# Kernel tuning notes

Hardware: AMD Instinct MI355X
Metric: run time of the kernel (lower is better)

The kernel has to match this reference:

```python
import jax, jax.numpy as jnp
import numpy as np

QMIN, QMAX = 0.0, 255.0  # uint8 affine quantization range


def _quant_dequant(x, scale, zero_point):
    # affine static quantization: q = clamp(round(x/scale) + zp, 0, 255)
    q = jnp.clip(jnp.round(x / scale) + zero_point, QMIN, QMAX)
    # dequantize back to float for the reference GEMM
    return (q - zero_point) * scale


def setup_inputs() -> dict:
    key = jax.random.key(0)
    k1, k2, k3, k4, k5 = jax.random.split(key, 5)
    N, IN, OUT = 4096, 4096, 4096
    x = jax.random.normal(k1, (N, IN), dtype=jnp.float32)
    weight = jax.random.normal(k2, (OUT, IN), dtype=jnp.float32) * 0.02
    bias = jax.random.normal(k3, (OUT,), dtype=jnp.float32)
    # static qparams (as produced by calculate_qparams of the observers)
    act_scale = jnp.float32(4.0 * 2.0 / 255.0)  # covers ~[-4, 4]
    act_zero_point = jnp.int32(128)
    weight_scale = (jax.random.uniform(k4, (OUT,), dtype=jnp.float32) * 0.5 + 0.5) * (0.08 * 2.0 / 255.0)
    weight_zero_point = jnp.full((OUT,), 128, dtype=jnp.int32)
    return {
        "x": x,
        "weight": weight,
        "bias": bias,
        "act_scale": act_scale,
        "act_zero_point": act_zero_point,
        "weight_scale": weight_scale,
        "weight_zero_point": weight_zero_point,
    }


def reference(x, weight, bias, act_scale, act_zero_point, weight_scale, weight_zero_point):
    # per-tensor static activation quantization
    x_dq = _quant_dequant(x, act_scale, act_zero_point.astype(jnp.float32))  # [N, in]
    # per-output-row weight quantization (block_size = (1, in_features))
    w_dq = _quant_dequant(
        weight,
        weight_scale[:, None],
        weight_zero_point.astype(jnp.float32)[:, None],
    )  # [out, in]
    # F.linear: x @ W^T + b
    return jnp.einsum("ni,oi->no", x_dq, w_dq) + bias
```

## Files before the change

kernel.cpp:

```cpp
#include <hip/hip_runtime.h>
#include <stdint.h>

typedef int   int4v   __attribute__((ext_vector_type(4)));
typedef float float4v __attribute__((ext_vector_type(4)));

static constexpr int DIM = 4096;
static constexpr int BT  = 128;
static constexpr int BK  = 128;
static constexpr int NKT = DIM / BK;

__global__ __launch_bounds__(256) void quant_act_kernel(
    const float* __restrict__ x, const float* __restrict__ s_ptr,
    const int* __restrict__ zp_ptr, int* __restrict__ out, int n4) {
  const float s  = s_ptr[0];
  const int   zp = zp_ptr[0];
  int idx    = blockIdx.x * blockDim.x + threadIdx.x;
  int stride = gridDim.x * blockDim.x;
  for (int i = idx; i < n4; i += stride) {
    float4v v = reinterpret_cast<const float4v*>(x)[i];
    int packed = 0;
#pragma unroll
    for (int j = 0; j < 4; ++j) {
      int q = (int)rintf(v[j] / s) + zp;
      q = min(max(q, 0), 255);
      q -= zp;
      packed |= (q & 255) << (8 * j);
    }
    out[i] = packed;
  }
}

__global__ __launch_bounds__(256) void quant_wgt_kernel(
    const float* __restrict__ w, const float* __restrict__ ws,
    const int* __restrict__ wzp, int* __restrict__ out, int n4) {
  int idx    = blockIdx.x * blockDim.x + threadIdx.x;
  int stride = gridDim.x * blockDim.x;
  for (int i = idx; i < n4; i += stride) {
    const int row = i >> 10;
    const float s = ws[row];
    const int  zp = wzp[row];
    float4v v = reinterpret_cast<const float4v*>(w)[i];
    int packed = 0;
#pragma unroll
    for (int j = 0; j < 4; ++j) {
      int q = (int)rintf(v[j] / s) + zp;
      q = min(max(q, 0), 255);
      q -= zp;
      packed |= (q & 255) << (8 * j);
    }
    out[i] = packed;
  }
}


__global__ __launch_bounds__(256, 2) void gemm_i8_w64(
    const signed char* __restrict__ A, const signed char* __restrict__ B,
    const float* __restrict__ s_act, const float* __restrict__ w_scale,
    const float* __restrict__ bias, float* __restrict__ C) {
  extern __shared__ signed char smem[];

  const int tid  = threadIdx.x;
  const int w    = tid >> 6;
  const int lane = tid & 63;
  const int wr = w >> 1, wc = w & 1;
  const int l15 = lane & 15, lhi = lane >> 4;
  const int swk = (l15 & 7) << 4;

  const int srow = lane >> 3;
  const int scol = ((lane & 7) ^ (lane >> 3)) << 4;

  const int tileM = blockIdx.y * BT;
  const int tileN = blockIdx.x * BT;

  auto stageA = [&](int i, int t) {
    signed char* dst = smem + (t & 1) * 32768;
    const int c = 4 * w + i;
    const size_t g = (size_t)(tileM + c * 8 + srow) * DIM + (size_t)t * BK + scol;
    __builtin_amdgcn_global_load_lds(
        (const __attribute__((address_space(1))) void*)(A + g),
        (__attribute__((address_space(3))) void*)(dst + c * 1024), 16, 0, 0);
  };
  auto stageB = [&](int i, int t) {
    signed char* dst = smem + (t & 1) * 32768 + 16384;
    const int c = 4 * w + i;
    const size_t g = (size_t)(tileN + c * 8 + srow) * DIM + (size_t)t * BK + scol;
    __builtin_amdgcn_global_load_lds(
        (const __attribute__((address_space(1))) void*)(B + g),
        (__attribute__((address_space(3))) void*)(dst + c * 1024), 16, 0, 0);
  };
  auto rdA = [&](const signed char* aL, int m, int kk) -> int4v {
    const int r = wr * 64 + m * 16 + l15;
    return *(const int4v*)(aL + r * BK + ((kk * 64 + lhi * 16) ^ swk));
  };
  auto rdB = [&](const signed char* bL, int n, int kk) -> int4v {
    const int r = wc * 64 + n * 16 + l15;
    return *(const int4v*)(bL + r * BK + ((kk * 64 + lhi * 16) ^ swk));
  };

  int4v acc[4][4] = {};
  int4v af[4][2];
  int4v bf[4][2];

#pragma unroll
  for (int i = 0; i < 4; ++i) { stageA(i, 0); stageB(i, 0); }
  asm volatile("s_waitcnt vmcnt(0)" ::: "memory");
  __builtin_amdgcn_s_barrier();

  for (int kt = 0; kt < NKT; ++kt) {
    const signed char* aC = smem + (kt & 1) * 32768;
    const signed char* bC = aC + 16384;

    if (kt + 1 < NKT) {
#pragma unroll
      for (int i = 0; i < 4; ++i) { stageA(i, kt + 1); stageB(i, kt + 1); }
    }

#pragma unroll
    for (int m = 0; m < 4; ++m) { af[m][0] = rdA(aC, m, 0); af[m][1] = rdA(aC, m, 1); }
#pragma unroll
    for (int n = 0; n < 4; ++n) { bf[n][0] = rdB(bC, n, 0); bf[n][1] = rdB(bC, n, 1); }

    __builtin_amdgcn_s_setprio(1);
#pragma unroll
    for (int kk = 0; kk < 2; ++kk)
#pragma unroll
      for (int m = 0; m < 4; ++m)
#pragma unroll
        for (int n = 0; n < 4; ++n)
          acc[m][n] = __builtin_amdgcn_mfma_i32_16x16x64_i8(
              af[m][kk], bf[n][kk], acc[m][n], 0, 0, 0);
    __builtin_amdgcn_s_setprio(0);

    asm volatile("s_waitcnt vmcnt(0)" ::: "memory");
    __builtin_amdgcn_s_barrier();
  }

  const float sa = s_act[0];
#pragma unroll
  for (int n = 0; n < 4; ++n) {
    const int col = tileN + wc * 64 + n * 16 + l15;
    const float sc = sa * w_scale[col];
    const float bs = bias[col];
#pragma unroll
    for (int m = 0; m < 4; ++m) {
      const int rbase = tileM + wr * 64 + m * 16 + lhi * 4;
#pragma unroll
      for (int j = 0; j < 4; ++j)
        C[(size_t)(rbase + j) * DIM + col] = (float)acc[m][n][j] * sc + bs;
    }
  }
}

extern "C" void kernel_launch(void* const* d_in, const int* in_sizes, int n_in,
                              void* d_out, int out_size, void* d_ws, size_t ws_size,
                              hipStream_t stream) {
  const float* x    = (const float*)d_in[0];
  const float* w    = (const float*)d_in[1];
  const float* bias = (const float*)d_in[2];
  const float* a_s  = (const float*)d_in[3];
  const int*   a_zp = (const int*)d_in[4];
  const float* w_s  = (const float*)d_in[5];
  const int*   w_zp = (const int*)d_in[6];
  float* out = (float*)d_out;

  signed char* a8 = (signed char*)d_ws;
  signed char* b8 = a8 + (size_t)DIM * DIM;

  const int n4 = DIM * DIM / 4;
  quant_act_kernel<<<2048, 256, 0, stream>>>(x, a_s, a_zp, (int*)a8, n4);
  quant_wgt_kernel<<<2048, 256, 0, stream>>>(w, w_s, w_zp, (int*)b8, n4);

  (void)hipFuncSetAttribute((const void*)gemm_i8_w64,
                            hipFuncAttributeMaxDynamicSharedMemorySize, 65536);
  dim3 grid(DIM / BT, DIM / BT);
  gemm_i8_w64<<<grid, 256, 65536, stream>>>(a8, b8, a_s, w_s, bias, out);
}
```

Before: 99.21 us.

## Halve GEMM K-tile to raise occupancy and fuse the two quantize kernels

```diff
diff --git a/kernel.cpp b/kernel.cpp
--- a/kernel.cpp
+++ b/kernel.cpp
@@ -6,18 +6,28 @@
 
 static constexpr int DIM = 4096;
 static constexpr int BT  = 128;
-static constexpr int BK  = 128;
+static constexpr int BK  = 64;
 static constexpr int NKT = DIM / BK;
 
-__global__ __launch_bounds__(256) void quant_act_kernel(
-    const float* __restrict__ x, const float* __restrict__ s_ptr,
-    const int* __restrict__ zp_ptr, int* __restrict__ out, int n4) {
-  const float s  = s_ptr[0];
-  const int   zp = zp_ptr[0];
-  int idx    = blockIdx.x * blockDim.x + threadIdx.x;
-  int stride = gridDim.x * blockDim.x;
+static constexpr int QB = 2048;
+
+__global__ __launch_bounds__(256) void quant_fused_kernel(
+    const float* __restrict__ x, const float* __restrict__ wgt,
+    const float* __restrict__ as_ptr, const int* __restrict__ azp_ptr,
+    const float* __restrict__ ws, const int* __restrict__ wzp,
+    int* __restrict__ a_out, int* __restrict__ b_out, int n4) {
+  const bool isAct = (blockIdx.x < QB);
+  const int  blk   = isAct ? blockIdx.x : blockIdx.x - QB;
+  const float* src = isAct ? x : wgt;
+  int* dst         = isAct ? a_out : b_out;
+  const float sAct = as_ptr[0];
+  const int   zpA  = azp_ptr[0];
+  int idx    = blk * blockDim.x + threadIdx.x;
+  int stride = QB * blockDim.x;
   for (int i = idx; i < n4; i += stride) {
-    float4v v = reinterpret_cast<const float4v*>(x)[i];
+    const float s = isAct ? sAct : ws[i >> 10];
+    const int  zp = isAct ? zpA  : wzp[i >> 10];
+    float4v v = reinterpret_cast<const float4v*>(src)[i];
     int packed = 0;
 #pragma unroll
     for (int j = 0; j < 4; ++j) {
@@ -26,34 +36,12 @@
       q -= zp;
       packed |= (q & 255) << (8 * j);
     }
-    out[i] = packed;
-  }
-}
-
-__global__ __launch_bounds__(256) void quant_wgt_kernel(
-    const float* __restrict__ w, const float* __restrict__ ws,
-    const int* __restrict__ wzp, int* __restrict__ out, int n4) {
-  int idx    = blockIdx.x * blockDim.x + threadIdx.x;
-  int stride = gridDim.x * blockDim.x;
-  for (int i = idx; i < n4; i += stride) {
-    const int row = i >> 10;
-    const float s = ws[row];
-    const int  zp = wzp[row];
-    float4v v = reinterpret_cast<const float4v*>(w)[i];
-    int packed = 0;
-#pragma unroll
-    for (int j = 0; j < 4; ++j) {
-      int q = (int)rintf(v[j] / s) + zp;
-      q = min(max(q, 0), 255);
-      q -= zp;
-      packed |= (q & 255) << (8 * j);
-    }
-    out[i] = packed;
+    dst[i] = packed;
   }
 }
 
 
-__global__ __launch_bounds__(256, 2) void gemm_i8_w64(
+__global__ __launch_bounds__(256, 5) void gemm_i8_bk64(
     const signed char* __restrict__ A, const signed char* __restrict__ B,
     const float* __restrict__ s_act, const float* __restrict__ w_scale,
     const float* __restrict__ bias, float* __restrict__ C) {
@@ -64,71 +52,67 @@
   const int lane = tid & 63;
   const int wr = w >> 1, wc = w & 1;
   const int l15 = lane & 15, lhi = lane >> 4;
-  const int swk = (l15 & 7) << 4;
+  const int swk = (l15 & 3) << 4;
 
-  const int srow = lane >> 3;
-  const int scol = ((lane & 7) ^ (lane >> 3)) << 4;
+  const int srow = lane >> 2;
+  const int scol = ((lane & 3) ^ (srow & 3)) << 4;
 
   const int tileM = blockIdx.y * BT;
   const int tileN = blockIdx.x * BT;
 
   auto stageA = [&](int i, int t) {
-    signed char* dst = smem + (t & 1) * 32768;
-    const int c = 4 * w + i;
-    const size_t g = (size_t)(tileM + c * 8 + srow) * DIM + (size_t)t * BK + scol;
+    signed char* dst = smem + (t & 1) * 16384;
+    const int c = 2 * w + i;
+    const size_t g = (size_t)(tileM + c * 16 + srow) * DIM + (size_t)t * BK + scol;
     __builtin_amdgcn_global_load_lds(
         (const __attribute__((address_space(1))) void*)(A + g),
         (__attribute__((address_space(3))) void*)(dst + c * 1024), 16, 0, 0);
   };
   auto stageB = [&](int i, int t) {
-    signed char* dst = smem + (t & 1) * 32768 + 16384;
-    const int c = 4 * w + i;
-    const size_t g = (size_t)(tileN + c * 8 + srow) * DIM + (size_t)t * BK + scol;
+    signed char* dst = smem + (t & 1) * 16384 + 8192;
+    const int c = 2 * w + i;
+    const size_t g = (size_t)(tileN + c * 16 + srow) * DIM + (size_t)t * BK + scol;
     __builtin_amdgcn_global_load_lds(
         (const __attribute__((address_space(1))) void*)(B + g),
         (__attribute__((address_space(3))) void*)(dst + c * 1024), 16, 0, 0);
   };
-  auto rdA = [&](const signed char* aL, int m, int kk) -> int4v {
+  auto rdA = [&](const signed char* aL, int m) -> int4v {
     const int r = wr * 64 + m * 16 + l15;
-    return *(const int4v*)(aL + r * BK + ((kk * 64 + lhi * 16) ^ swk));
+    return *(const int4v*)(aL + r * BK + ((lhi * 16) ^ swk));
   };
-  auto rdB = [&](const signed char* bL, int n, int kk) -> int4v {
+  auto rdB = [&](const signed char* bL, int n) -> int4v {
     const int r = wc * 64 + n * 16 + l15;
-    return *(const int4v*)(bL + r * BK + ((kk * 64 + lhi * 16) ^ swk));
+    return *(const int4v*)(bL + r * BK + ((lhi * 16) ^ swk));
   };
 
   int4v acc[4][4] = {};
-  int4v af[4][2];
-  int4v bf[4][2];
+  int4v af[4], bf[4];
 
-#pragma unroll
-  for (int i = 0; i < 4; ++i) { stageA(i, 0); stageB(i, 0); }
+  stageA(0, 0); stageA(1, 0); stageB(0, 0); stageB(1, 0);
   asm volatile("s_waitcnt vmcnt(0)" ::: "memory");
   __builtin_amdgcn_s_barrier();
 
   for (int kt = 0; kt < NKT; ++kt) {
-    const signed char* aC = smem + (kt & 1) * 32768;
-    const signed char* bC = aC + 16384;
+    const signed char* aC = smem + (kt & 1) * 16384;
+    const signed char* bC = aC + 8192;
 
     if (kt + 1 < NKT) {
-#pragma unroll
-      for (int i = 0; i < 4; ++i) { stageA(i, kt + 1); stageB(i, kt + 1); }
+      stageA(0, kt + 1); stageA(1, kt + 1);
+      stageB(0, kt + 1); stageB(1, kt + 1);
     }
 
 #pragma unroll
-    for (int m = 0; m < 4; ++m) { af[m][0] = rdA(aC, m, 0); af[m][1] = rdA(aC, m, 1); }
+    for (int m = 0; m < 4; ++m) af[m] = rdA(aC, m);
 #pragma unroll
-    for (int n = 0; n < 4; ++n) { bf[n][0] = rdB(bC, n, 0); bf[n][1] = rdB(bC, n, 1); }
+    for (int n = 0; n < 4; ++n) bf[n] = rdB(bC, n);
 
     __builtin_amdgcn_s_setprio(1);
 #pragma unroll
-    for (int kk = 0; kk < 2; ++kk)
+    for (int m = 0; m < 4; ++m)
 #pragma unroll
-      for (int m = 0; m < 4; ++m)
-#pragma unroll
-        for (int n = 0; n < 4; ++n)
-          acc[m][n] = __builtin_amdgcn_mfma_i32_16x16x64_i8(
-              af[m][kk], bf[n][kk], acc[m][n], 0, 0, 0);
+      for (int n = 0; n < 4; ++n)
+        acc[m][n] = __builtin_amdgcn_mfma_i32_16x16x64_i8(
+            af[m], bf[n], acc[m][n], 0, 0, 0);
     __builtin_amdgcn_s_setprio(0);
 
     asm volatile("s_waitcnt vmcnt(0)" ::: "memory");
@@ -167,11 +151,11 @@
   signed char* b8 = a8 + (size_t)DIM * DIM;
 
   const int n4 = DIM * DIM / 4;
-  quant_act_kernel<<<2048, 256, 0, stream>>>(x, a_s, a_zp, (int*)a8, n4);
-  quant_wgt_kernel<<<2048, 256, 0, stream>>>(w, w_s, w_zp, (int*)b8, n4);
+  quant_fused_kernel<<<2 * QB, 256, 0, stream>>>(x, w, a_s, a_zp, w_s, w_zp,
+                                                 (int*)a8, (int*)b8, n4);
 
-  (void)hipFuncSetAttribute((const void*)gemm_i8_w64,
-                            hipFuncAttributeMaxDynamicSharedMemorySize, 65536);
+  (void)hipFuncSetAttribute((const void*)gemm_i8_bk64,
+                            hipFuncAttributeMaxDynamicSharedMemorySize, 32768);
   dim3 grid(DIM / BT, DIM / BT);
-  gemm_i8_w64<<<grid, 256, 65536, stream>>>(a8, b8, a_s, w_s, bias, out);
+  gemm_i8_bk64<<<grid, 256, 32768, stream>>>(a8, b8, a_s, w_s, bias, out);
 }
```

Result: slower. 336.7 us (+239.4%).

## Pre-pack weight into MFMA fragment layout and load B directly from global

Applied to the files above, without the earlier changes.

```diff
diff --git a/kernel.cpp b/kernel.cpp
--- a/kernel.cpp
+++ b/kernel.cpp
@@ -30,31 +30,42 @@
   }
 }
 
-__global__ __launch_bounds__(256) void quant_wgt_kernel(
+__global__ __launch_bounds__(256) void quant_wgt_frag(
     const float* __restrict__ w, const float* __restrict__ ws,
-    const int* __restrict__ wzp, int* __restrict__ out, int n4) {
-  int idx    = blockIdx.x * blockDim.x + threadIdx.x;
-  int stride = gridDim.x * blockDim.x;
-  for (int i = idx; i < n4; i += stride) {
-    const int row = i >> 10;
+    const int* __restrict__ wzp, int4v* __restrict__ bp) {
+  const int t    = threadIdx.x;
+  const int wv   = t >> 6, lane = t & 63;
+  const int l15  = lane & 15, lhi = lane >> 4;
+  const int NFRAG = (DIM / 16) * NKT * 2;
+  for (int f = blockIdx.x * 4 + wv; f < NFRAG; f += gridDim.x * 4) {
+    const int row16 = f >> 6;
+    const int rem   = f & 63;
+    const int kt    = rem >> 1, kk = rem & 1;
+    const int row   = row16 * 16 + l15;
+    const int col   = kt * 128 + kk * 64 + lhi * 16;
     const float s = ws[row];
     const int  zp = wzp[row];
-    float4v v = reinterpret_cast<const float4v*>(w)[i];
-    int packed = 0;
+    int4v q;
 #pragma unroll
-    for (int j = 0; j < 4; ++j) {
-      int q = (int)rintf(v[j] / s) + zp;
-      q = min(max(q, 0), 255);
-      q -= zp;
-      packed |= (q & 255) << (8 * j);
+    for (int v4 = 0; v4 < 4; ++v4) {
+      float4v xv = *reinterpret_cast<const float4v*>(w + (size_t)row * DIM + col + v4 * 4);
+      int packed = 0;
+#pragma unroll
+      for (int j = 0; j < 4; ++j) {
+        int qq = (int)rintf(xv[j] / s) + zp;
+        qq = min(max(qq, 0), 255);
+        qq -= zp;
+        packed |= (qq & 255) << (8 * j);
+      }
+      q[v4] = packed;
     }
-    out[i] = packed;
+    bp[(size_t)f * 64 + lane] = q;
   }
 }
 
 
-__global__ __launch_bounds__(256, 2) void gemm_i8_w64(
-    const signed char* __restrict__ A, const signed char* __restrict__ B,
+__global__ __launch_bounds__(256, 3) void gemm_i8_bdir(
+    const signed char* __restrict__ A, const int4v* __restrict__ Bp,
     const float* __restrict__ s_act, const float* __restrict__ w_scale,
     const float* __restrict__ bias, float* __restrict__ C) {
   extern __shared__ signed char smem[];
@@ -71,30 +82,23 @@
 
   const int tileM = blockIdx.y * BT;
   const int tileN = blockIdx.x * BT;
+  const int rb16  = (tileN >> 4) + wc * 4;
 
   auto stageA = [&](int i, int t) {
-    signed char* dst = smem + (t & 1) * 32768;
+    signed char* dst = smem + (t & 1) * 16384;
     const int c = 4 * w + i;
     const size_t g = (size_t)(tileM + c * 8 + srow) * DIM + (size_t)t * BK + scol;
     __builtin_amdgcn_global_load_lds(
         (const __attribute__((address_space(1))) void*)(A + g),
         (__attribute__((address_space(3))) void*)(dst + c * 1024), 16, 0, 0);
   };
-  auto stageB = [&](int i, int t) {
-    signed char* dst = smem + (t & 1) * 32768 + 16384;
-    const int c = 4 * w + i;
-    const size_t g = (size_t)(tileN + c * 8 + srow) * DIM + (size_t)t * BK + scol;
-    __builtin_amdgcn_global_load_lds(
-        (const __attribute__((address_space(1))) void*)(B + g),
-        (__attribute__((address_space(3))) void*)(dst + c * 1024), 16, 0, 0);
-  };
   auto rdA = [&](const signed char* aL, int m, int kk) -> int4v {
     const int r = wr * 64 + m * 16 + l15;
     return *(const int4v*)(aL + r * BK + ((kk * 64 + lhi * 16) ^ swk));
   };
-  auto rdB = [&](const signed char* bL, int n, int kk) -> int4v {
-    const int r = wc * 64 + n * 16 + l15;
-    return *(const int4v*)(bL + r * BK + ((kk * 64 + lhi * 16) ^ swk));
+  auto ldB = [&](int n, int kt, int kk) -> int4v {
+    const size_t f = ((size_t)(rb16 + n) * NKT + kt) * 2 + kk;
+    return Bp[f * 64 + lane];
   };
 
   int4v acc[4][4] = {};
@@ -102,23 +106,23 @@
   int4v bf[4][2];
 
 #pragma unroll
-  for (int i = 0; i < 4; ++i) { stageA(i, 0); stageB(i, 0); }
+  for (int i = 0; i < 4; ++i) stageA(i, 0);
   asm volatile("s_waitcnt vmcnt(0)" ::: "memory");
   __builtin_amdgcn_s_barrier();
 
   for (int kt = 0; kt < NKT; ++kt) {
-    const signed char* aC = smem + (kt & 1) * 32768;
-    const signed char* bC = aC + 16384;
+    const signed char* aC = smem + (kt & 1) * 16384;
+
+#pragma unroll
+    for (int n = 0; n < 4; ++n) { bf[n][0] = ldB(n, kt, 0); bf[n][1] = ldB(n, kt, 1); }
 
     if (kt + 1 < NKT) {
 #pragma unroll
-      for (int i = 0; i < 4; ++i) { stageA(i, kt + 1); stageB(i, kt + 1); }
+      for (int i = 0; i < 4; ++i) stageA(i, kt + 1);
     }
 
 #pragma unroll
     for (int m = 0; m < 4; ++m) { af[m][0] = rdA(aC, m, 0); af[m][1] = rdA(aC, m, 1); }
-#pragma unroll
-    for (int n = 0; n < 4; ++n) { bf[n][0] = rdB(bC, n, 0); bf[n][1] = rdB(bC, n, 1); }
 
     __builtin_amdgcn_s_setprio(1);
 #pragma unroll
@@ -164,14 +168,14 @@
   float* out = (float*)d_out;
 
   signed char* a8 = (signed char*)d_ws;
-  signed char* b8 = a8 + (size_t)DIM * DIM;
+  int4v*       bp = (int4v*)(a8 + (size_t)DIM * DIM);
 
   const int n4 = DIM * DIM / 4;
   quant_act_kernel<<<2048, 256, 0, stream>>>(x, a_s, a_zp, (int*)a8, n4);
-  quant_wgt_kernel<<<2048, 256, 0, stream>>>(w, w_s, w_zp, (int*)b8, n4);
+  quant_wgt_frag<<<2048, 256, 0, stream>>>(w, w_s, w_zp, bp);
 
-  (void)hipFuncSetAttribute((const void*)gemm_i8_w64,
-                            hipFuncAttributeMaxDynamicSharedMemorySize, 65536);
+  (void)hipFuncSetAttribute((const void*)gemm_i8_bdir,
+                            hipFuncAttributeMaxDynamicSharedMemorySize, 32768);
   dim3 grid(DIM / BT, DIM / BT);
-  gemm_i8_w64<<<grid, 256, 65536, stream>>>(a8, b8, a_s, w_s, bias, out);
+  gemm_i8_bdir<<<grid, 256, 32768, stream>>>(a8, bp, a_s, w_s, bias, out);
 }
```

New measurement: 114.6 us. 15.5% more time.
